# Optimization experiments

Measured on AMD Instinct MI355X. Metric: run time of the kernel, lower is better.

The kernel has to match this reference:

```python
import jax, jax.numpy as jnp
import numpy as np

B, G, NPA, NT, L = 8192, 689, 16, 131, 6
S = G + NPA * NT  # 2785 = 689 genes + 16 nodes per each of 131 assemblies


def setup_inputs() -> dict:
    key = jax.random.key(0)
    ks = jax.random.split(key, 8)
    x = jax.random.normal(ks[0], (B, G), dtype=jnp.float32)
    # depth-0 mask: place the 689 gene inputs into the first 689 slots of the layer
    lm0 = jnp.zeros((G, S), jnp.float32).at[jnp.arange(G), jnp.arange(G)].set(1.0)
    # per-depth sparse binary connectivity masks (ontology DAG edges at each depth)
    lm = (jax.random.uniform(ks[1], (L, S, S)) < 0.02).astype(jnp.float32)
    # diagonal pass-through masks for edges skipping this depth (stored as diagonals)
    flm_diag = (jax.random.uniform(ks[2], (L, S)) < 0.3).astype(jnp.float32)
    # final assembly selector: the nodes_per_assembly slots of the root assembly
    fasm = jnp.zeros((S,), jnp.float32).at[G:G + NPA].set(1.0)
    W0 = jax.random.normal(ks[3], (G, S), dtype=jnp.float32) * 0.05
    b0 = jnp.zeros((S,), jnp.float32)
    W = jax.random.normal(ks[4], (L, S, S), dtype=jnp.float32) * 0.05
    b = jnp.zeros((L, S), jnp.float32)
    gamma = jnp.ones((L + 1, S), jnp.float32)
    beta = jnp.zeros((L + 1, S), jnp.float32)
    w_out = jax.random.normal(ks[5], (S,), dtype=jnp.float32) * 0.05
    b_out = jnp.zeros((), jnp.float32)
    return {"x": x, "lm0": lm0, "lm": lm, "flm_diag": flm_diag, "fasm": fasm,
            "W0": W0, "b0": b0, "W": W, "b": b, "gamma": gamma, "beta": beta,
            "w_out": w_out, "b_out": b_out}


def _bn(h, g, bt, eps=1e-5):
    # training-mode BatchNorm1d over the batch axis
    m = h.mean(axis=0)
    v = h.var(axis=0)
    return (h - m) * jax.lax.rsqrt(v + eps) * g + bt


def reference(x, lm0, lm, flm_diag, fasm, W0, b0, W, b, gamma, beta, w_out, b_out):
    # depth 0: masked linear placing genes into layer slots, BN before activation
    h = jnp.tanh(_bn(x @ (W0 * lm0) + b0, gamma[0], beta[0]))  # [B, S]
    def step(h, layer):
        Wl, bl, lml, dl, gl, btl = layer
        # masked linear + BN + activation, plus diagonal pass-through skip
        hn = jnp.tanh(_bn(h @ (Wl * lml) + bl, gl, btl)) + h * dl
        return hn, None
    h, _ = jax.lax.scan(step, h, (W, b, lm, flm_diag, gamma[1:], beta[1:]))
    # output_method='final': linear head on final-assembly nodes only
    return (h * fasm) @ w_out + b_out  # [B]
```

## Files before the change

kernel.cpp:

```cpp
#include <hip/hip_runtime.h>
#include <hip/hip_fp16.h>
#include <stdint.h>

typedef uint32_t u32;
typedef unsigned int v4u __attribute__((ext_vector_type(4)));

constexpr int CB   = 8192;
constexpr int CG   = 689;
constexpr int CL   = 6;
constexpr int CS   = 2785;
constexpr int CSP  = 2816;
constexpr int CRS  = 8256;
constexpr int KCAP = 128;

union V16 { v4u u; __half2 h2[4]; };

__global__ __launch_bounds__(256) void build_main(const float* __restrict__ lm,
                                                  const float* __restrict__ W,
                                                  u32* __restrict__ entries,
                                                  int* __restrict__ cnt)
{
    int i = blockIdx.x * 256 + threadIdx.x;
    const int total = CL * CS * CS;
    if (i >= total) return;
    float m = lm[i];
    if (m != 0.0f) {
        int s = i % CS;
        int r = i / CS;
        int l = r / CS;
        int j = r % CS;
        float w = W[i] * m;
        int col = (l + 1) * CSP + s;
        int pos = atomicAdd(&cnt[col], 1);
        if (pos < KCAP) {
            unsigned short hw = __half_as_ushort(__float2half(w));
            entries[col * KCAP + pos] = ((u32)j << 16) | (u32)hw;
        }
    }
}

__global__ __launch_bounds__(256) void build0(const float* __restrict__ lm0,
                                              const float* __restrict__ W0,
                                              u32* __restrict__ entries,
                                              int* __restrict__ cnt)
{
    int i = blockIdx.x * 256 + threadIdx.x;
    const int total = CG * CS;
    if (i >= total) return;
    float m = lm0[i];
    if (m != 0.0f) {
        int s = i % CS;
        int j = i / CS;
        float w = W0[i] * m;
        int pos = atomicAdd(&cnt[s], 1);
        if (pos < KCAP) {
            unsigned short hw = __half_as_ushort(__float2half(w));
            entries[s * KCAP + pos] = ((u32)j << 16) | (u32)hw;
        }
    }
}

__global__ __launch_bounds__(256) void transpose_x(const float* __restrict__ x,
                                                   __half* __restrict__ xT)
{
    __shared__ float tile[32][33];
    int gx = blockIdx.x * 32;
    int gy = blockIdx.y * 32;
    int tx = threadIdx.x, ty = threadIdx.y;
#pragma unroll
    for (int i = 0; i < 32; i += 8) {
        int g = gx + tx;
        int b = gy + ty + i;
        tile[ty + i][tx] = (g < CG) ? x[(size_t)b * CG + g] : 0.f;
    }
    __syncthreads();
#pragma unroll
    for (int i = 0; i < 32; i += 8) {
        int g = gx + ty + i;
        int b = gy + tx;
        if (g < CG) xT[(size_t)g * CRS + b] = __float2half(tile[tx][ty + i]);
    }
}

__global__ __launch_bounds__(64) void gather_k(const __half* __restrict__ src,
                                               __half* __restrict__ dst,
                                               const u32* __restrict__ entries,
                                               const int* __restrict__ cnt,
                                               const float* __restrict__ bias,
                                               float* __restrict__ sumv,
                                               float* __restrict__ sumq,
                                               int boff0)
{
    int s = blockIdx.y;
    int boff = boff0 + blockIdx.x * 512 + threadIdx.x * 8;
    int n = cnt[s];
    if (n > KCAP) n = KCAP;
    const u32* e = entries + s * KCAP;
    float bs = bias[s];
    float acc[8];
#pragma unroll
    for (int j = 0; j < 8; j++) acc[j] = bs;

    int k = 0;
    for (; k + 4 <= n; k += 4) {
        v4u ee = *reinterpret_cast<const v4u*>(e + k);
        u32 evs[4] = {ee.x, ee.y, ee.z, ee.w};
#pragma unroll
        for (int q = 0; q < 4; q++) {
            u32 ev = evs[q];
            int idx = (int)(ev >> 16);
            float w = __half2float(__ushort_as_half((unsigned short)(ev & 0xffffu)));
            V16 v; v.u = *reinterpret_cast<const v4u*>(src + (size_t)idx * CRS + boff);
#pragma unroll
            for (int j = 0; j < 4; j++) {
                float2 f = __half22float2(v.h2[j]);
                acc[2*j]   = fmaf(w, f.x, acc[2*j]);
                acc[2*j+1] = fmaf(w, f.y, acc[2*j+1]);
            }
        }
    }
    for (; k < n; k++) {
        u32 ev = e[k];
        int idx = (int)(ev >> 16);
        float w = __half2float(__ushort_as_half((unsigned short)(ev & 0xffffu)));
        V16 v; v.u = *reinterpret_cast<const v4u*>(src + (size_t)idx * CRS + boff);
#pragma unroll
        for (int j = 0; j < 4; j++) {
            float2 f = __half22float2(v.h2[j]);
            acc[2*j]   = fmaf(w, f.x, acc[2*j]);
            acc[2*j+1] = fmaf(w, f.y, acc[2*j+1]);
        }
    }

    V16 o;
#pragma unroll
    for (int j = 0; j < 4; j++) o.h2[j] = __floats2half2_rn(acc[2*j], acc[2*j+1]);
    __builtin_nontemporal_store(o.u, reinterpret_cast<v4u*>(dst + (size_t)s * CRS + boff));

    float ls = 0.f, lq = 0.f;
#pragma unroll
    for (int j = 0; j < 8; j++) { ls += acc[j]; lq += acc[j] * acc[j]; }
#pragma unroll
    for (int off = 32; off > 0; off >>= 1) {
        ls += __shfl_xor(ls, off);
        lq += __shfl_xor(lq, off);
    }
    if (threadIdx.x == 0) { atomicAdd(&sumv[s], ls); atomicAdd(&sumq[s], lq); }
}

__global__ __launch_bounds__(256) void bn_act(__half* __restrict__ h,
                                              const __half* __restrict__ prev,
                                              const float* __restrict__ sumv,
                                              const float* __restrict__ sumq,
                                              const float* __restrict__ gamma,
                                              const float* __restrict__ beta,
                                              const float* __restrict__ dlv)
{
    int s = blockIdx.y;
    int boff = blockIdx.x * 2048 + threadIdx.x * 8;
    float mean = sumv[s] * (1.0f / CB);
    float var  = sumq[s] * (1.0f / CB) - mean * mean;
    float rstd = rsqrtf(var + 1e-5f);
    float scale = gamma[s] * rstd;
    float shift = beta[s] - mean * scale;
    size_t base = (size_t)s * CRS + boff;
    V16 v; v.u = *reinterpret_cast<const v4u*>(h + base);
    V16 pv;
    float d = 0.f;
    if (prev) { d = dlv[s]; pv.u = *reinterpret_cast<const v4u*>(prev + base); }
    V16 o;
#pragma unroll
    for (int j = 0; j < 4; j++) {
        float2 f = __half22float2(v.h2[j]);
        float t0 = tanhf(fmaf(f.x, scale, shift));
        float t1 = tanhf(fmaf(f.y, scale, shift));
        if (prev) {
            float2 p = __half22float2(pv.h2[j]);
            t0 = fmaf(d, p.x, t0);
            t1 = fmaf(d, p.y, t1);
        }
        o.h2[j] = __floats2half2_rn(t0, t1);
    }
    *reinterpret_cast<v4u*>(h + base) = o.u;
}

__global__ __launch_bounds__(256) void head_k(const __half* __restrict__ h,
                                              const float* __restrict__ fasm,
                                              const float* __restrict__ wout,
                                              const float* __restrict__ bout,
                                              float* __restrict__ out)
{
    int b = blockIdx.x * 256 + threadIdx.x;
    int seg = blockIdx.y;
    int s0 = seg * 349;
    int s1 = s0 + 349; if (s1 > CS) s1 = CS;
    float acc = (seg == 0) ? bout[0] : 0.f;
    for (int s = s0; s < s1; s++) {
        float wv = fasm[s] * wout[s];
        if (wv != 0.f) acc = fmaf(wv, __half2float(h[(size_t)s * CRS + b]), acc);
    }
    atomicAdd(&out[b], acc);
}

extern "C" void kernel_launch(void* const* d_in, const int* in_sizes, int n_in,
                              void* d_out, int out_size, void* d_ws, size_t ws_size,
                              hipStream_t stream)
{
    const float* x    = (const float*)d_in[0];
    const float* lm0  = (const float*)d_in[1];
    const float* lm   = (const float*)d_in[2];
    const float* flm  = (const float*)d_in[3];
    const float* fasm = (const float*)d_in[4];
    const float* W0   = (const float*)d_in[5];
    const float* b0   = (const float*)d_in[6];
    const float* W    = (const float*)d_in[7];
    const float* bb   = (const float*)d_in[8];
    const float* gam  = (const float*)d_in[9];
    const float* bet  = (const float*)d_in[10];
    const float* wout = (const float*)d_in[11];
    const float* bout = (const float*)d_in[12];
    float* out = (float*)d_out;

    char* ws = (char*)d_ws;
    int*    cnt     = (int*)ws;
    float*  sumv    = (float*)(ws + 78848);
    float*  sumq    = (float*)(ws + 157696);
    u32*    entries = (u32*)(ws + 236544);
    __half* xT      = (__half*)(ws + 10329088);
    __half* hA      = (__half*)(ws + 21705856);
    __half* hB      = (__half*)(ws + 67691776);

    (void)hipMemsetAsync(ws, 0, 236544, stream);
    (void)hipMemsetAsync(d_out, 0, (size_t)out_size * sizeof(float), stream);

    { int total = CL * CS * CS; build_main<<<dim3((total + 255) / 256), 256, 0, stream>>>(lm, W, entries, cnt); }
    { int total = CG * CS;      build0   <<<dim3((total + 255) / 256), 256, 0, stream>>>(lm0, W0, entries, cnt); }
    transpose_x<<<dim3(22, 256), dim3(32, 8), 0, stream>>>(x, xT);

    const __half* cur = xT;
    __half* bufs[2] = {hA, hB};
    int which = 0;
    for (int t = 0; t < 7; t++) {
        __half* dst = bufs[which];
        const float* bias = (t == 0) ? b0 : bb + (size_t)(t - 1) * CS;
        for (int half = 0; half < 2; half++) {
            gather_k<<<dim3(8, CS), 64, 0, stream>>>(cur, dst,
                entries + (size_t)t * CSP * KCAP, cnt + t * CSP, bias,
                sumv + t * CSP, sumq + t * CSP, half * 4096);
        }
        bn_act<<<dim3(4, CS), 256, 0, stream>>>(dst, (t == 0) ? nullptr : cur,
            sumv + t * CSP, sumq + t * CSP, gam + (size_t)t * CS, bet + (size_t)t * CS,
            (t == 0) ? nullptr : flm + (size_t)(t - 1) * CS);
        cur = dst;
        which ^= 1;
    }
    head_k<<<dim3(32, 8), 256, 0, stream>>>(cur, fasm, wout, bout, out);
}
```

Baseline: 1.443 ms.

## Software-pipeline sparse gather with 64-bit byte-offset entries and vectorized build

Sparse entries become 64-bit: a precomputed byte offset into the source plus an fp32 weight. The gather kernel processes them in groups of eight and prefetches the next group's entries and source rows while the current group is accumulated. The whole entry table is zero-filled so padded slots contribute nothing. The build kernels now read mask and weights with float4 loads. bn_act uses 64-thread blocks, the head kernel writes its outputs directly, which drops the atomics and the output memset, and the x transpose now lives in the second ping-pong buffer. In exchange the entry table doubles in bytes per entry, the per-column capacity drops to 112, the memset is much larger, and the prefetch needs more registers and reads padding rows.

```diff
diff --git a/kernel.cpp b/kernel.cpp
--- a/kernel.cpp
+++ b/kernel.cpp
@@ -3,6 +3,7 @@
 #include <stdint.h>
 
 typedef uint32_t u32;
+typedef uint64_t u64;
 typedef unsigned int v4u __attribute__((ext_vector_type(4)));
 
 constexpr int CB   = 8192;
@@ -11,51 +12,83 @@
 constexpr int CS   = 2785;
 constexpr int CSP  = 2816;
 constexpr int CRS  = 8256;
-constexpr int KCAP = 128;
+constexpr int KCAP = 112;
 
 union V16 { v4u u; __half2 h2[4]; };
 
 __global__ __launch_bounds__(256) void build_main(const float* __restrict__ lm,
                                                   const float* __restrict__ W,
-                                                  u32* __restrict__ entries,
+                                                  u64* __restrict__ ent,
                                                   int* __restrict__ cnt)
 {
-    int i = blockIdx.x * 256 + threadIdx.x;
     const int total = CL * CS * CS;
-    if (i >= total) return;
-    float m = lm[i];
-    if (m != 0.0f) {
-        int s = i % CS;
-        int r = i / CS;
-        int l = r / CS;
-        int j = r % CS;
-        float w = W[i] * m;
-        int col = (l + 1) * CSP + s;
-        int pos = atomicAdd(&cnt[col], 1);
-        if (pos < KCAP) {
-            unsigned short hw = __half_as_ushort(__float2half(w));
-            entries[col * KCAP + pos] = ((u32)j << 16) | (u32)hw;
+    int base = (blockIdx.x * 256 + threadIdx.x) * 16;
+#pragma unroll
+    for (int c = 0; c < 16; c += 4) {
+        int i4 = base + c;
+        if (i4 >= total) break;
+        float mm[4], ww[4];
+        if (i4 + 4 <= total) {
+            float4 m4 = *reinterpret_cast<const float4*>(lm + i4);
+            float4 w4 = *reinterpret_cast<const float4*>(W + i4);
+            mm[0]=m4.x; mm[1]=m4.y; mm[2]=m4.z; mm[3]=m4.w;
+            ww[0]=w4.x; ww[1]=w4.y; ww[2]=w4.z; ww[3]=w4.w;
+        } else {
+            for (int q = 0; q < 4; q++) {
+                mm[q] = (i4 + q < total) ? lm[i4 + q] : 0.f;
+                ww[q] = (i4 + q < total) ? W[i4 + q]  : 0.f;
+            }
+        }
+#pragma unroll
+        for (int q = 0; q < 4; q++) {
+            if (mm[q] != 0.0f) {
+                int i = i4 + q;
+                int s = i % CS;
+                int r = i / CS;
+                int l = r / CS;
+                int j = r % CS;
+                int col = l * CSP + s;
+                int pos = atomicAdd(&cnt[col], 1);
+                if (pos < KCAP) {
+                    u32 off = (u32)j * (u32)(CRS * 2);
+                    ent[(size_t)col * KCAP + pos] = ((u64)off << 32) | (u64)__float_as_uint(ww[q]);
+                }
+            }
         }
     }
 }
 
 __global__ __launch_bounds__(256) void build0(const float* __restrict__ lm0,
                                               const float* __restrict__ W0,
-                                              u32* __restrict__ entries,
+                                              u64* __restrict__ ent,
                                               int* __restrict__ cnt)
 {
-    int i = blockIdx.x * 256 + threadIdx.x;
     const int total = CG * CS;
-    if (i >= total) return;
-    float m = lm0[i];
-    if (m != 0.0f) {
-        int s = i % CS;
-        int j = i / CS;
-        float w = W0[i] * m;
-        int pos = atomicAdd(&cnt[s], 1);
-        if (pos < KCAP) {
-            unsigned short hw = __half_as_ushort(__float2half(w));
-            entries[s * KCAP + pos] = ((u32)j << 16) | (u32)hw;
+    int i4 = (blockIdx.x * 256 + threadIdx.x) * 4;
+    if (i4 >= total) return;
+    float mm[4], ww[4];
+    if (i4 + 4 <= total) {
+        float4 m4 = *reinterpret_cast<const float4*>(lm0 + i4);
+        float4 w4 = *reinterpret_cast<const float4*>(W0 + i4);
+        mm[0]=m4.x; mm[1]=m4.y; mm[2]=m4.z; mm[3]=m4.w;
+        ww[0]=w4.x; ww[1]=w4.y; ww[2]=w4.z; ww[3]=w4.w;
+    } else {
+        for (int q = 0; q < 4; q++) {
+            mm[q] = (i4 + q < total) ? lm0[i4 + q] : 0.f;
+            ww[q] = (i4 + q < total) ? W0[i4 + q]  : 0.f;
+        }
+    }
+#pragma unroll
+    for (int q = 0; q < 4; q++) {
+        if (mm[q] != 0.0f) {
+            int i = i4 + q;
+            int s = i % CS;
+            int j = i / CS;
+            int pos = atomicAdd(&cnt[s], 1);
+            if (pos < KCAP) {
+                u32 off = (u32)j * (u32)(CRS * 2);
+                ent[(size_t)s * KCAP + pos] = ((u64)off << 32) | (u64)__float_as_uint(ww[q]);
+            }
         }
     }
 }
@@ -84,51 +117,58 @@
 
 __global__ __launch_bounds__(64) void gather_k(const __half* __restrict__ src,
                                                __half* __restrict__ dst,
-                                               const u32* __restrict__ entries,
+                                               const u64* __restrict__ ent,
                                                const int* __restrict__ cnt,
                                                const float* __restrict__ bias,
                                                float* __restrict__ sumv,
                                                float* __restrict__ sumq,
                                                int boff0)
 {
-    int s = blockIdx.y;
-    int boff = boff0 + blockIdx.x * 512 + threadIdx.x * 8;
-    int n = cnt[s];
-    if (n > KCAP) n = KCAP;
-    const u32* e = entries + s * KCAP;
-    float bs = bias[s];
+    int s    = blockIdx.y;
+    int lane = threadIdx.x;
+    int boff = boff0 + blockIdx.x * 512 + lane * 8;
+
+    int n = cnt[s]; if (n > KCAP) n = KCAP;
+    int ng = (n + 7) >> 3;
+    const u64* e = ent + (size_t)s * KCAP;
+    const char* sb = (const char*)src + (size_t)boff * 2;
+
+    float bv = bias[s];
     float acc[8];
 #pragma unroll
-    for (int j = 0; j < 8; j++) acc[j] = bs;
-
-    int k = 0;
-    for (; k + 4 <= n; k += 4) {
-        v4u ee = *reinterpret_cast<const v4u*>(e + k);
-        u32 evs[4] = {ee.x, ee.y, ee.z, ee.w};
-#pragma unroll
-        for (int q = 0; q < 4; q++) {
-            u32 ev = evs[q];
-            int idx = (int)(ev >> 16);
-            float w = __half2float(__ushort_as_half((unsigned short)(ev & 0xffffu)));
-            V16 v; v.u = *reinterpret_cast<const v4u*>(src + (size_t)idx * CRS + boff);
+    for (int j = 0; j < 8; j++) acc[j] = bv;
+
+    u64 ev[8]; V16 rv[8];
+    if (ng > 0) {
+#pragma unroll
+        for (int q = 0; q < 8; q++) {
+            ev[q] = e[q];
+            rv[q].u = *reinterpret_cast<const v4u*>(sb + (ev[q] >> 32));
+        }
+    }
+    for (int g = 0; g < ng; g++) {
+        u64 en[8]; V16 rn[8];
+        bool more = (g + 1 < ng);
+        if (more) {
+#pragma unroll
+            for (int q = 0; q < 8; q++) {
+                en[q] = e[(g + 1) * 8 + q];
+                rn[q].u = *reinterpret_cast<const v4u*>(sb + (en[q] >> 32));
+            }
+        }
+#pragma unroll
+        for (int q = 0; q < 8; q++) {
+            float w = __uint_as_float((u32)(ev[q] & 0xffffffffu));
 #pragma unroll
             for (int j = 0; j < 4; j++) {
-                float2 f = __half22float2(v.h2[j]);
+                float2 f = __half22float2(rv[q].h2[j]);
                 acc[2*j]   = fmaf(w, f.x, acc[2*j]);
                 acc[2*j+1] = fmaf(w, f.y, acc[2*j+1]);
             }
         }
-    }
-    for (; k < n; k++) {
-        u32 ev = e[k];
-        int idx = (int)(ev >> 16);
-        float w = __half2float(__ushort_as_half((unsigned short)(ev & 0xffffu)));
-        V16 v; v.u = *reinterpret_cast<const v4u*>(src + (size_t)idx * CRS + boff);
-#pragma unroll
-        for (int j = 0; j < 4; j++) {
-            float2 f = __half22float2(v.h2[j]);
-            acc[2*j]   = fmaf(w, f.x, acc[2*j]);
-            acc[2*j+1] = fmaf(w, f.y, acc[2*j+1]);
+        if (more) {
+#pragma unroll
+            for (int q = 0; q < 8; q++) { ev[q] = en[q]; rv[q] = rn[q]; }
         }
     }
 
@@ -145,19 +185,19 @@
         ls += __shfl_xor(ls, off);
         lq += __shfl_xor(lq, off);
     }
-    if (threadIdx.x == 0) { atomicAdd(&sumv[s], ls); atomicAdd(&sumq[s], lq); }
-}
-
-__global__ __launch_bounds__(256) void bn_act(__half* __restrict__ h,
-                                              const __half* __restrict__ prev,
-                                              const float* __restrict__ sumv,
-                                              const float* __restrict__ sumq,
-                                              const float* __restrict__ gamma,
-                                              const float* __restrict__ beta,
-                                              const float* __restrict__ dlv)
+    if (lane == 0) { atomicAdd(&sumv[s], ls); atomicAdd(&sumq[s], lq); }
+}
+
+__global__ __launch_bounds__(64) void bn_act(__half* __restrict__ h,
+                                             const __half* __restrict__ prev,
+                                             const float* __restrict__ sumv,
+                                             const float* __restrict__ sumq,
+                                             const float* __restrict__ gamma,
+                                             const float* __restrict__ beta,
+                                             const float* __restrict__ dlv)
 {
     int s = blockIdx.y;
-    int boff = blockIdx.x * 2048 + threadIdx.x * 8;
+    int boff = blockIdx.x * 512 + threadIdx.x * 8;
     float mean = sumv[s] * (1.0f / CB);
     float var  = sumq[s] * (1.0f / CB) - mean * mean;
     float rstd = rsqrtf(var + 1e-5f);
@@ -190,16 +230,25 @@
                                               const float* __restrict__ bout,
                                               float* __restrict__ out)
 {
-    int b = blockIdx.x * 256 + threadIdx.x;
-    int seg = blockIdx.y;
-    int s0 = seg * 349;
-    int s1 = s0 + 349; if (s1 > CS) s1 = CS;
-    float acc = (seg == 0) ? bout[0] : 0.f;
-    for (int s = s0; s < s1; s++) {
-        float wv = fasm[s] * wout[s];
-        if (wv != 0.f) acc = fmaf(wv, __half2float(h[(size_t)s * CRS + b]), acc);
-    }
-    atomicAdd(&out[b], acc);
+    int b = (blockIdx.x * 256 + threadIdx.x) * 8;
+    float bo = bout[0];
+    float acc[8];
+#pragma unroll
+    for (int j = 0; j < 8; j++) acc[j] = bo;
+    for (int s = 0; s < CS; s++) {
+        float c = fasm[s] * wout[s];
+        if (c != 0.f) {
+            V16 v; v.u = *reinterpret_cast<const v4u*>(h + (size_t)s * CRS + b);
+#pragma unroll
+            for (int j = 0; j < 4; j++) {
+                float2 f = __half22float2(v.h2[j]);
+                acc[2*j]   = fmaf(c, f.x, acc[2*j]);
+                acc[2*j+1] = fmaf(c, f.y, acc[2*j+1]);
+            }
+        }
+    }
+    *reinterpret_cast<float4*>(out + b)     = make_float4(acc[0], acc[1], acc[2], acc[3]);
+    *reinterpret_cast<float4*>(out + b + 4) = make_float4(acc[4], acc[5], acc[6], acc[7]);
 }
 
 extern "C" void kernel_launch(void* const* d_in, const int* in_sizes, int n_in,
@@ -222,19 +271,18 @@
     float* out = (float*)d_out;
 
     char* ws = (char*)d_ws;
-    int*    cnt     = (int*)ws;
-    float*  sumv    = (float*)(ws + 78848);
-    float*  sumq    = (float*)(ws + 157696);
-    u32*    entries = (u32*)(ws + 236544);
-    __half* xT      = (__half*)(ws + 10329088);
-    __half* hA      = (__half*)(ws + 21705856);
-    __half* hB      = (__half*)(ws + 67691776);
-
-    (void)hipMemsetAsync(ws, 0, 236544, stream);
-    (void)hipMemsetAsync(d_out, 0, (size_t)out_size * sizeof(float), stream);
-
-    { int total = CL * CS * CS; build_main<<<dim3((total + 255) / 256), 256, 0, stream>>>(lm, W, entries, cnt); }
-    { int total = CG * CS;      build0   <<<dim3((total + 255) / 256), 256, 0, stream>>>(lm0, W0, entries, cnt); }
+    int*    cnt  = (int*)ws;
+    float*  sumv = (float*)(ws + 78848);
+    float*  sumq = (float*)(ws + 157696);
+    u64*    ent  = (u64*)(ws + 236544);
+    __half* hA   = (__half*)(ws + 17898496);
+    __half* hB   = (__half*)(ws + 63884416);
+    __half* xT   = hB;
+
+    (void)hipMemsetAsync(ws, 0, 17898496, stream);
+
+    { int total = CL * CS * CS; build_main<<<dim3((total + 4095) / 4096), 256, 0, stream>>>(lm, W, ent + (size_t)CSP * KCAP, cnt + CSP); }
+    { int total = CG * CS;      build0   <<<dim3((total + 1023) / 1024), 256, 0, stream>>>(lm0, W0, ent, cnt); }
     transpose_x<<<dim3(22, 256), dim3(32, 8), 0, stream>>>(x, xT);
 
     const __half* cur = xT;
@@ -245,14 +293,14 @@
         const float* bias = (t == 0) ? b0 : bb + (size_t)(t - 1) * CS;
         for (int half = 0; half < 2; half++) {
             gather_k<<<dim3(8, CS), 64, 0, stream>>>(cur, dst,
-                entries + (size_t)t * CSP * KCAP, cnt + t * CSP, bias,
+                ent + (size_t)t * CSP * KCAP, cnt + t * CSP, bias,
                 sumv + t * CSP, sumq + t * CSP, half * 4096);
         }
-        bn_act<<<dim3(4, CS), 256, 0, stream>>>(dst, (t == 0) ? nullptr : cur,
+        bn_act<<<dim3(16, CS), 64, 0, stream>>>(dst, (t == 0) ? nullptr : cur,
             sumv + t * CSP, sumq + t * CSP, gam + (size_t)t * CS, bet + (size_t)t * CS,
             (t == 0) ? nullptr : flm + (size_t)(t - 1) * CS);
         cur = dst;
         which ^= 1;
     }
-    head_k<<<dim3(32, 8), 256, 0, stream>>>(cur, fasm, wout, bout, out);
-}
+    head_k<<<dim3(4, 1), 256, 0, stream>>>(cur, fasm, wout, bout, out);
+}
```

Result: slower. 1.926 ms (+33.4%).
